# Performance work log

Hardware: AMD Instinct MI355X
Metric: run time of the kernel (lower is better)

Reference implementation:

```python
import math
import jax, jax.numpy as jnp
import numpy as np

# Frozen random shifts from the original module's __init__ (random.randint(-1,1))
SHIFT_C = 1   # p_2_0_1: roll along channel dim
SHIFT_H = 1   # p_4_1_0: roll along h
SHIFT_W = -1  # p_4_1_1: roll along w
K = 7         # horizontal window size (F.unfold kernel (1,7), padding (0,3))


def setup_inputs() -> dict:
    key = jax.random.key(0)
    k1, k2 = jax.random.split(key)
    n, c, h, w = 8, 256, 56, 56
    x = jax.random.normal(k1, (n, c, h, w), dtype=jnp.float32)
    # p_1_w ~ trunc_normal(std=0.1) around 1.0; approximate with 1 + 0.1*normal
    p1w = 1.0 + 0.1 * jax.random.normal(k2, (1, c, h, w), dtype=jnp.float32)
    return {"x": x, "p1w": p1w}


def _unfold_w7(t):
    # t: (n,c,h,w) -> (n,c,7,h,w): 7 horizontal taps, zero-padded (pad=3)
    w = t.shape[-1]
    tp = jnp.pad(t, ((0, 0), (0, 0), (0, 0), (3, 3)))
    return jnp.stack([tp[..., j:j + w] for j in range(K)], axis=2)


def reference(x, p1w):
    n, c, h, w = x.shape
    hw = h * w
    t1 = p1w * x                              # (n,c,h,w)
    t2 = jnp.roll(t1, SHIFT_C, axis=1)        # roll channels
    t3 = _unfold_w7(t2)                       # (n,c,7,h,w)
    t4 = jnp.roll(jnp.roll(t3, SHIFT_H, axis=3), SHIFT_W, axis=4)
    t5 = t1[:, :, None] - t3                  # (n,c,7,h,w)
    t6 = x[:, :, None] + t4                   # (n,c,7,h,w)
    x2 = x.reshape(n, c, hw)
    t5r = t5.reshape(n, c, K, hw)
    t6r = t6.reshape(n, c, K, hw)
    # scores: bmm(x (n,c,hw), t5^T (n,hw,c*7)) -> (n,c,c,7)
    t7 = jnp.einsum('nip,njkp->nijk', x2, t5r) / math.sqrt(hw)
    # aggregate: bmm(t7 (n,c,c*7), t6 (n,c*7,hw)) -> (n,c,hw)
    t8 = jnp.einsum('nijk,njkp->nip', t7, t6r) / math.sqrt(c * K)
    return t8.reshape(n, c, h, w)
```

## Files before the change

kernel.cpp:

```cpp
#include <hip/hip_runtime.h>

typedef unsigned short u16;
typedef __bf16 bf16x8 __attribute__((ext_vector_type(8)));
typedef float f32x4 __attribute__((ext_vector_type(4)));

#define HH  56
#define WW  56
#define HW  3136
#define CC  256
#define NB  8
#define CKP 2048
#define KS1 4
#define KS2 2

__device__ __forceinline__ u16 f2bf(float f) {
  unsigned int u = __float_as_uint(f);
  u += 0x7fffu + ((u >> 16) & 1u);
  return (u16)(u >> 16);
}
__device__ __forceinline__ float bf2f(u16 v) {
  return __uint_as_float((unsigned)v << 16);
}

__device__ __forceinline__ void lds_load16(const void* g, void* l) {
  __builtin_amdgcn_global_load_lds(
      (const __attribute__((address_space(1))) void*)g,
      (__attribute__((address_space(3))) void*)l, 16, 0, 0);
}

__global__ void pass1(const float* __restrict__ x, const float* __restrict__ p1w,
                      u16* __restrict__ t1b, u16* __restrict__ xb) {
  int i = blockIdx.x * 256 + threadIdx.x;
  int cw = i % (CC * HW / 4);
  float4 xv = ((const float4*)x)[i];
  float4 wv = ((const float4*)p1w)[cw];
  uint2 xo = make_uint2((unsigned)f2bf(xv.x) | ((unsigned)f2bf(xv.y) << 16),
                        (unsigned)f2bf(xv.z) | ((unsigned)f2bf(xv.w) << 16));
  ((uint2*)xb)[i] = xo;
  uint2 to = make_uint2((unsigned)f2bf(xv.x * wv.x) | ((unsigned)f2bf(xv.y * wv.y) << 16),
                        (unsigned)f2bf(xv.z * wv.z) | ((unsigned)f2bf(xv.w * wv.w) << 16));
  ((uint2*)t1b)[i] = to;
}

__global__ __launch_bounds__(256)
void gemm1f(const u16* __restrict__ A, const u16* __restrict__ t1b,
            float* __restrict__ Cp) {
  __shared__ u16 As[128 * 64];
  __shared__ u16 Bs[128 * 64];

  const int z = blockIdx.z, nb = z / KS1, ks = z % KS1;
  const int it0 = 49 * ks / KS1, it1 = 49 * (ks + 1) / KS1;
  const u16* Ab  = A   + (long)nb * CC * HW;
  const u16* t1n = t1b + (long)nb * CC * HW;
  const int m0 = blockIdx.x * 128, n0 = blockIdx.y * 128;
  const int jb = blockIdx.y * 16;
  const int t = threadIdx.x;
  const int lane = t & 63, wave = t >> 6;
  const int wm = wave & 1, wn = wave >> 1;
  const int lm = lane & 15, quad = lane >> 4;

  const int jl = (t >> 3) & 15, pc = t & 7, hf = t >> 7;
  const int j  = jb + jl;
  const int jm = (j + CC - 1) & (CC - 1);
  const u16* arow = t1n + (long)j  * HW;
  const u16* wrow = t1n + (long)jm * HW;

  f32x4 acc[4][4];
#pragma unroll
  for (int a = 0; a < 4; ++a)
#pragma unroll
    for (int b = 0; b < 4; ++b) acc[a][b] = (f32x4)0.0f;

  int rowc[4], colc[4];
#pragma unroll
  for (int ci = 0; ci < 4; ++ci) {
    int c = t + ci * 256;
    rowc[ci] = c >> 3;
    colc[ci] = ((c & 7) ^ (rowc[ci] & 7)) * 8;
  }

  for (int it = it0; it < it1; ++it) {
    const int k0 = it * 64;
#pragma unroll
    for (int ci = 0; ci < 4; ++ci)
      lds_load16(Ab + (long)(m0 + rowc[ci]) * HW + k0 + colc[ci],
                 &As[(t + ci * 256) * 8]);

    {
      const int p8 = k0 + pc * 8;
      u16 Ar[8], Wd[24];
      *(uint4*)Ar = *(const uint4*)&arow[p8];
#pragma unroll
      for (int L = 0; L < 3; ++L) {
        int ad = p8 - 8 + L * 8;
        ad = ad < 0 ? 0 : (ad > HW - 8 ? HW - 8 : ad);
        *(uint4*)&Wd[L * 8] = *(const uint4*)&wrow[ad];
      }
      int w0t = p8 % 56;
      float Af[8];
#pragma unroll
      for (int e = 0; e < 8; ++e) Af[e] = bf2f(Ar[e]);
      if (hf == 0) {
#pragma unroll
        for (int k = 0; k < 4; ++k) {
          u16 v[8];
#pragma unroll
          for (int e = 0; e < 8; ++e) {
            int w = w0t + e; if (w >= 56) w -= 56;
            float tap = ((unsigned)(w + k - 3) < 56u) ? bf2f(Wd[e + k + 5]) : 0.f;
            v[e] = f2bf(Af[e] - tap);
          }
          *(uint4*)&Bs[(jl * 8 + k) * 64 + (pc ^ k) * 8] = make_uint4(
              v[0] | ((unsigned)v[1] << 16), v[2] | ((unsigned)v[3] << 16),
              v[4] | ((unsigned)v[5] << 16), v[6] | ((unsigned)v[7] << 16));
        }
      } else {
#pragma unroll
        for (int k = 4; k < 7; ++k) {
          u16 v[8];
#pragma unroll
          for (int e = 0; e < 8; ++e) {
            int w = w0t + e; if (w >= 56) w -= 56;
            float tap = ((unsigned)(w + k - 3) < 56u) ? bf2f(Wd[e + k + 5]) : 0.f;
            v[e] = f2bf(Af[e] - tap);
          }
          *(uint4*)&Bs[(jl * 8 + k) * 64 + (pc ^ k) * 8] = make_uint4(
              v[0] | ((unsigned)v[1] << 16), v[2] | ((unsigned)v[3] << 16),
              v[4] | ((unsigned)v[5] << 16), v[6] | ((unsigned)v[7] << 16));
        }
        *(uint4*)&Bs[(jl * 8 + 7) * 64 + (pc ^ 7) * 8] = make_uint4(0, 0, 0, 0);
      }
    }
    __syncthreads();
#pragma unroll
    for (int kk = 0; kk < 2; ++kk) {
      const int phys = ((kk * 4 + quad) ^ (lm & 7)) * 8;
      bf16x8 af[4], bv[4];
#pragma unroll
      for (int mi = 0; mi < 4; ++mi)
        af[mi] = *(const bf16x8*)&As[(wm * 64 + mi * 16 + lm) * 64 + phys];
#pragma unroll
      for (int ni = 0; ni < 4; ++ni)
        bv[ni] = *(const bf16x8*)&Bs[(wn * 64 + ni * 16 + lm) * 64 + phys];
#pragma unroll
      for (int mi = 0; mi < 4; ++mi)
#pragma unroll
        for (int ni = 0; ni < 4; ++ni)
          acc[mi][ni] = __builtin_amdgcn_mfma_f32_16x16x32_bf16(
              af[mi], bv[ni], acc[mi][ni], 0, 0, 0);
    }
    __syncthreads();
  }

  float* Cb = Cp + ((long)ks * NB + nb) * (long)CC * CKP;
#pragma unroll
  for (int mi = 0; mi < 4; ++mi)
#pragma unroll
    for (int ni = 0; ni < 4; ++ni) {
      int rb = m0 + wm * 64 + mi * 16 + quad * 4;
      int cg = n0 + wn * 64 + ni * 16 + lm;
#pragma unroll
      for (int r = 0; r < 4; ++r)
        Cb[(long)(rb + r) * CKP + cg] = acc[mi][ni][r];
    }
}

__global__ void reduce1(const float* __restrict__ p1, u16* __restrict__ t7) {
  const int i = blockIdx.x * 256 + threadIdx.x;
  const long S = (long)NB * CC * CKP / 4;
  float4 a = ((const float4*)p1)[i];
  float4 b = ((const float4*)p1)[i + S];
  float4 c = ((const float4*)p1)[i + 2 * S];
  float4 d = ((const float4*)p1)[i + 3 * S];
  const float s = 1.0f / 56.0f;
  float e0 = (a.x + b.x + c.x + d.x) * s;
  float e1 = (a.y + b.y + c.y + d.y) * s;
  float e2 = (a.z + b.z + c.z + d.z) * s;
  float e3 = (a.w + b.w + c.w + d.w) * s;
  u16 w3 = (i & 1) ? (u16)0 : f2bf(e3);
  ushort4 o = make_ushort4(f2bf(e0), f2bf(e1), f2bf(e2), w3);
  ((ushort4*)t7)[i] = o;
}

__global__ __launch_bounds__(256)
void gemm2f(const u16* __restrict__ A, const u16* __restrict__ xb,
            const u16* __restrict__ t1b, float* __restrict__ Cp) {
  __shared__ u16 As[128 * 64];
  __shared__ u16 Bs[64 * 64];

  const int z = blockIdx.z, nb = z / KS2, ks = z % KS2;
  const int it0 = 16 * ks, it1 = 16 * (ks + 1);
  const u16* Ab  = A   + (long)nb * CC * CKP;
  const u16* xbn = xb  + (long)nb * CC * HW;
  const u16* t1n = t1b + (long)nb * CC * HW;
  const int m0 = blockIdx.x * 128, n0 = blockIdx.y * 64;
  const int t = threadIdx.x;
  const int lane = t & 63, wave = t >> 6;
  const int wm = wave & 1, wn = wave >> 1;
  const int lm = lane & 15, quad = lane >> 4;

  const int pr = t & 63, jg = t >> 6;
  const int p  = n0 + pr;
  const int h  = p / WW, w = p - h * WW;
  const int h2 = (h + HH - 1) % HH;
  const int w2 = (w + 1) % WW;
  const int swz = pr & 7;

  f32x4 acc[4][2];
#pragma unroll
  for (int a = 0; a < 4; ++a)
#pragma unroll
    for (int b = 0; b < 2; ++b) acc[a][b] = (f32x4)0.0f;

  int rowc[4], colc[4];
#pragma unroll
  for (int ci = 0; ci < 4; ++ci) {
    int c = t + ci * 256;
    rowc[ci] = c >> 3;
    colc[ci] = ((c & 7) ^ (rowc[ci] & 7)) * 8;
  }

  for (int it = it0; it < it1; ++it) {
    const int k0 = it * 64;
#pragma unroll
    for (int ci = 0; ci < 4; ++ci)
      lds_load16(Ab + (long)(m0 + rowc[ci]) * CKP + k0 + colc[ci],
                 &As[(t + ci * 256) * 8]);

#pragma unroll
    for (int jj = 0; jj < 2; ++jj) {
      const int jch = it * 8 + jg * 2 + jj;
      const int jmm = (jch + CC - 1) & (CC - 1);
      const float xv = bf2f(xbn[(long)jch * HW + p]);
      const u16* trow = t1n + (long)jmm * HW + h2 * WW;
      u16 v[8];
#pragma unroll
      for (int k = 0; k < 7; ++k) {
        int ww = w2 + k - 3;
        int wc = ww < 0 ? 0 : (ww > 55 ? 55 : ww);
        float tv = bf2f(trow[wc]);
        float tap = ((unsigned)ww < 56u) ? tv : 0.f;
        v[k] = f2bf(xv + tap);
      }
      v[7] = 0;
      *(uint4*)&Bs[pr * 64 + (((jg * 2 + jj) ^ swz) * 8)] = make_uint4(
          v[0] | ((unsigned)v[1] << 16), v[2] | ((unsigned)v[3] << 16),
          v[4] | ((unsigned)v[5] << 16), v[6] | ((unsigned)v[7] << 16));
    }
    __syncthreads();
#pragma unroll
    for (int kk = 0; kk < 2; ++kk) {
      const int phys = ((kk * 4 + quad) ^ (lm & 7)) * 8;
      bf16x8 af[4], bv[2];
#pragma unroll
      for (int mi = 0; mi < 4; ++mi)
        af[mi] = *(const bf16x8*)&As[(wm * 64 + mi * 16 + lm) * 64 + phys];
#pragma unroll
      for (int ni = 0; ni < 2; ++ni)
        bv[ni] = *(const bf16x8*)&Bs[(wn * 32 + ni * 16 + lm) * 64 + phys];
#pragma unroll
      for (int mi = 0; mi < 4; ++mi)
#pragma unroll
        for (int ni = 0; ni < 2; ++ni)
          acc[mi][ni] = __builtin_amdgcn_mfma_f32_16x16x32_bf16(
              af[mi], bv[ni], acc[mi][ni], 0, 0, 0);
    }
    __syncthreads();
  }

  float* Cb = Cp + ((long)ks * NB + nb) * (long)CC * HW;
#pragma unroll
  for (int mi = 0; mi < 4; ++mi)
#pragma unroll
    for (int ni = 0; ni < 2; ++ni) {
      int rb = m0 + wm * 64 + mi * 16 + quad * 4;
      int cg = n0 + wn * 32 + ni * 16 + lm;
#pragma unroll
      for (int r = 0; r < 4; ++r)
        Cb[(long)(rb + r) * HW + cg] = acc[mi][ni][r];
    }
}

__global__ void reduce2(const float* __restrict__ p2, float* __restrict__ out) {
  const int i = blockIdx.x * 256 + threadIdx.x;
  const long S = (long)NB * CC * HW / 4;
  float4 a = ((const float4*)p2)[i];
  float4 b = ((const float4*)p2)[i + S];
  const float s = 0.023622783f;
  float4 o;
  o.x = (a.x + b.x) * s; o.y = (a.y + b.y) * s;
  o.z = (a.z + b.z) * s; o.w = (a.w + b.w) * s;
  ((float4*)out)[i] = o;
}

extern "C" void kernel_launch(void* const* d_in, const int* in_sizes, int n_in,
                              void* d_out, int out_size, void* d_ws, size_t ws_size,
                              hipStream_t stream) {
  const float* x   = (const float*)d_in[0];
  const float* p1w = (const float*)d_in[1];

  char* ws = (char*)d_ws;
  size_t o = 0;
  u16* xb  = (u16*)(ws + o); o += (size_t)NB * CC * HW * 2;
  u16* t1b = (u16*)(ws + o); o += (size_t)NB * CC * HW * 2;
  u16* t7  = (u16*)(ws + o); o += (size_t)NB * CC * CKP * 2;
  float* p1 = (float*)(ws + o); o += (size_t)KS1 * NB * CC * CKP * 4;
  float* p2 = p1;

  pass1<<<NB * CC * HW / 4 / 256, 256, 0, stream>>>(x, p1w, t1b, xb);
  gemm1f<<<dim3(2, 16, NB * KS1), 256, 0, stream>>>(xb, t1b, p1);
  reduce1<<<NB * CC * CKP / 4 / 256, 256, 0, stream>>>(p1, t7);
  gemm2f<<<dim3(2, 49, NB * KS2), 256, 0, stream>>>(t7, xb, t1b, p2);
  reduce2<<<NB * CC * HW / 4 / 256, 256, 0, stream>>>(p2, (float*)d_out);
}
```

Measured before the change: 216.0 us.

## Double-buffer generated B tiles and read A fragments directly from global

Both GEMM kernels now keep the on-the-fly generated B operand in a double-buffered LDS tile. The next tile is generated after the current MFMA step, so only one barrier per iteration is needed and generation can overlap the matrix math. The A operand is no longer staged through LDS with global_load_lds; each wave loads its bf16x8 fragments straight from global memory. This frees LDS and removes the staging traffic, but risks uncoalesced, repeated global reads of A across the waves that share rows, relying on L1/L2 caches.

```diff
diff --git a/kernel.cpp b/kernel.cpp
--- a/kernel.cpp
+++ b/kernel.cpp
@@ -20,12 +20,6 @@
 }
 __device__ __forceinline__ float bf2f(u16 v) {
   return __uint_as_float((unsigned)v << 16);
-}
-
-__device__ __forceinline__ void lds_load16(const void* g, void* l) {
-  __builtin_amdgcn_global_load_lds(
-      (const __attribute__((address_space(1))) void*)g,
-      (__attribute__((address_space(3))) void*)l, 16, 0, 0);
 }
 
 __global__ void pass1(const float* __restrict__ x, const float* __restrict__ p1w,
@@ -45,8 +39,7 @@
 __global__ __launch_bounds__(256)
 void gemm1f(const u16* __restrict__ A, const u16* __restrict__ t1b,
             float* __restrict__ Cp) {
-  __shared__ u16 As[128 * 64];
-  __shared__ u16 Bs[128 * 64];
+  __shared__ u16 Bs[2 * 128 * 64];
 
   const int z = blockIdx.z, nb = z / KS1, ks = z % KS1;
   const int it0 = 49 * ks / KS1, it1 = 49 * (ks + 1) / KS1;
@@ -71,77 +64,71 @@
 #pragma unroll
     for (int b = 0; b < 4; ++b) acc[a][b] = (f32x4)0.0f;
 
-  int rowc[4], colc[4];
-#pragma unroll
-  for (int ci = 0; ci < 4; ++ci) {
-    int c = t + ci * 256;
-    rowc[ci] = c >> 3;
-    colc[ci] = ((c & 7) ^ (rowc[ci] & 7)) * 8;
-  }
+  auto genB = [&](int it, int buf) {
+    const int k0 = it * 64;
+    const int p8 = k0 + pc * 8;
+    u16* Bp = &Bs[buf * 8192];
+    u16 Ar[8], Wd[24];
+    *(uint4*)Ar = *(const uint4*)&arow[p8];
+#pragma unroll
+    for (int L = 0; L < 3; ++L) {
+      int ad = p8 - 8 + L * 8;
+      ad = ad < 0 ? 0 : (ad > HW - 8 ? HW - 8 : ad);
+      *(uint4*)&Wd[L * 8] = *(const uint4*)&wrow[ad];
+    }
+    int w0t = p8 % 56;
+    float Af[8];
+#pragma unroll
+    for (int e = 0; e < 8; ++e) Af[e] = bf2f(Ar[e]);
+    if (hf == 0) {
+#pragma unroll
+      for (int k = 0; k < 4; ++k) {
+        u16 v[8];
+#pragma unroll
+        for (int e = 0; e < 8; ++e) {
+          int w = w0t + e; if (w >= 56) w -= 56;
+          float tap = ((unsigned)(w + k - 3) < 56u) ? bf2f(Wd[e + k + 5]) : 0.f;
+          v[e] = f2bf(Af[e] - tap);
+        }
+        *(uint4*)&Bp[(jl * 8 + k) * 64 + (pc ^ k) * 8] = make_uint4(
+            v[0] | ((unsigned)v[1] << 16), v[2] | ((unsigned)v[3] << 16),
+            v[4] | ((unsigned)v[5] << 16), v[6] | ((unsigned)v[7] << 16));
+      }
+    } else {
+#pragma unroll
+      for (int k = 4; k < 7; ++k) {
+        u16 v[8];
+#pragma unroll
+        for (int e = 0; e < 8; ++e) {
+          int w = w0t + e; if (w >= 56) w -= 56;
+          float tap = ((unsigned)(w + k - 3) < 56u) ? bf2f(Wd[e + k + 5]) : 0.f;
+          v[e] = f2bf(Af[e] - tap);
+        }
+        *(uint4*)&Bp[(jl * 8 + k) * 64 + (pc ^ k) * 8] = make_uint4(
+            v[0] | ((unsigned)v[1] << 16), v[2] | ((unsigned)v[3] << 16),
+            v[4] | ((unsigned)v[5] << 16), v[6] | ((unsigned)v[7] << 16));
+      }
+      *(uint4*)&Bp[(jl * 8 + 7) * 64 + (pc ^ 7) * 8] = make_uint4(0, 0, 0, 0);
+    }
+  };
+
+  genB(it0, 0);
+  __syncthreads();
 
   for (int it = it0; it < it1; ++it) {
     const int k0 = it * 64;
-#pragma unroll
-    for (int ci = 0; ci < 4; ++ci)
-      lds_load16(Ab + (long)(m0 + rowc[ci]) * HW + k0 + colc[ci],
-                 &As[(t + ci * 256) * 8]);
-
-    {
-      const int p8 = k0 + pc * 8;
-      u16 Ar[8], Wd[24];
-      *(uint4*)Ar = *(const uint4*)&arow[p8];
-#pragma unroll
-      for (int L = 0; L < 3; ++L) {
-        int ad = p8 - 8 + L * 8;
-        ad = ad < 0 ? 0 : (ad > HW - 8 ? HW - 8 : ad);
-        *(uint4*)&Wd[L * 8] = *(const uint4*)&wrow[ad];
-      }
-      int w0t = p8 % 56;
-      float Af[8];
-#pragma unroll
-      for (int e = 0; e < 8; ++e) Af[e] = bf2f(Ar[e]);
-      if (hf == 0) {
-#pragma unroll
-        for (int k = 0; k < 4; ++k) {
-          u16 v[8];
-#pragma unroll
-          for (int e = 0; e < 8; ++e) {
-            int w = w0t + e; if (w >= 56) w -= 56;
-            float tap = ((unsigned)(w + k - 3) < 56u) ? bf2f(Wd[e + k + 5]) : 0.f;
-            v[e] = f2bf(Af[e] - tap);
-          }
-          *(uint4*)&Bs[(jl * 8 + k) * 64 + (pc ^ k) * 8] = make_uint4(
-              v[0] | ((unsigned)v[1] << 16), v[2] | ((unsigned)v[3] << 16),
-              v[4] | ((unsigned)v[5] << 16), v[6] | ((unsigned)v[7] << 16));
-        }
-      } else {
-#pragma unroll
-        for (int k = 4; k < 7; ++k) {
-          u16 v[8];
-#pragma unroll
-          for (int e = 0; e < 8; ++e) {
-            int w = w0t + e; if (w >= 56) w -= 56;
-            float tap = ((unsigned)(w + k - 3) < 56u) ? bf2f(Wd[e + k + 5]) : 0.f;
-            v[e] = f2bf(Af[e] - tap);
-          }
-          *(uint4*)&Bs[(jl * 8 + k) * 64 + (pc ^ k) * 8] = make_uint4(
-              v[0] | ((unsigned)v[1] << 16), v[2] | ((unsigned)v[3] << 16),
-              v[4] | ((unsigned)v[5] << 16), v[6] | ((unsigned)v[7] << 16));
-        }
-        *(uint4*)&Bs[(jl * 8 + 7) * 64 + (pc ^ 7) * 8] = make_uint4(0, 0, 0, 0);
-      }
-    }
-    __syncthreads();
+    const int cb = (it - it0) & 1;
 #pragma unroll
     for (int kk = 0; kk < 2; ++kk) {
       const int phys = ((kk * 4 + quad) ^ (lm & 7)) * 8;
       bf16x8 af[4], bv[4];
 #pragma unroll
       for (int mi = 0; mi < 4; ++mi)
-        af[mi] = *(const bf16x8*)&As[(wm * 64 + mi * 16 + lm) * 64 + phys];
+        af[mi] = *(const bf16x8*)&Ab[(long)(m0 + wm * 64 + mi * 16 + lm) * HW
+                                     + k0 + (kk * 4 + quad) * 8];
 #pragma unroll
       for (int ni = 0; ni < 4; ++ni)
-        bv[ni] = *(const bf16x8*)&Bs[(wn * 64 + ni * 16 + lm) * 64 + phys];
+        bv[ni] = *(const bf16x8*)&Bs[cb * 8192 + (wn * 64 + ni * 16 + lm) * 64 + phys];
 #pragma unroll
       for (int mi = 0; mi < 4; ++mi)
 #pragma unroll
@@ -149,6 +136,8 @@
           acc[mi][ni] = __builtin_amdgcn_mfma_f32_16x16x32_bf16(
               af[mi], bv[ni], acc[mi][ni], 0, 0, 0);
     }
+    int itn = it + 1 < it1 ? it + 1 : it;
+    genB(itn, cb ^ 1);
     __syncthreads();
   }
 
@@ -185,8 +174,7 @@
 __global__ __launch_bounds__(256)
 void gemm2f(const u16* __restrict__ A, const u16* __restrict__ xb,
             const u16* __restrict__ t1b, float* __restrict__ Cp) {
-  __shared__ u16 As[128 * 64];
-  __shared__ u16 Bs[64 * 64];
+  __shared__ u16 Bs[2 * 64 * 64];
 
   const int z = blockIdx.z, nb = z / KS2, ks = z % KS2;
   const int it0 = 16 * ks, it1 = 16 * (ks + 1);
@@ -212,21 +200,8 @@
 #pragma unroll
     for (int b = 0; b < 2; ++b) acc[a][b] = (f32x4)0.0f;
 
-  int rowc[4], colc[4];
-#pragma unroll
-  for (int ci = 0; ci < 4; ++ci) {
-    int c = t + ci * 256;
-    rowc[ci] = c >> 3;
-    colc[ci] = ((c & 7) ^ (rowc[ci] & 7)) * 8;
-  }
-
-  for (int it = it0; it < it1; ++it) {
-    const int k0 = it * 64;
-#pragma unroll
-    for (int ci = 0; ci < 4; ++ci)
-      lds_load16(Ab + (long)(m0 + rowc[ci]) * CKP + k0 + colc[ci],
-                 &As[(t + ci * 256) * 8]);
-
+  auto genB = [&](int it, int buf) {
+    u16* Bp = &Bs[buf * 4096];
 #pragma unroll
     for (int jj = 0; jj < 2; ++jj) {
       const int jch = it * 8 + jg * 2 + jj;
@@ -243,21 +218,29 @@
         v[k] = f2bf(xv + tap);
       }
       v[7] = 0;
-      *(uint4*)&Bs[pr * 64 + (((jg * 2 + jj) ^ swz) * 8)] = make_uint4(
+      *(uint4*)&Bp[pr * 64 + (((jg * 2 + jj) ^ swz) * 8)] = make_uint4(
           v[0] | ((unsigned)v[1] << 16), v[2] | ((unsigned)v[3] << 16),
           v[4] | ((unsigned)v[5] << 16), v[6] | ((unsigned)v[7] << 16));
     }
-    __syncthreads();
+  };
+
+  genB(it0, 0);
+  __syncthreads();
+
+  for (int it = it0; it < it1; ++it) {
+    const int k0 = it * 64;
+    const int cb = (it - it0) & 1;
 #pragma unroll
     for (int kk = 0; kk < 2; ++kk) {
       const int phys = ((kk * 4 + quad) ^ (lm & 7)) * 8;
       bf16x8 af[4], bv[2];
 #pragma unroll
       for (int mi = 0; mi < 4; ++mi)
-        af[mi] = *(const bf16x8*)&As[(wm * 64 + mi * 16 + lm) * 64 + phys];
+        af[mi] = *(const bf16x8*)&Ab[(long)(m0 + wm * 64 + mi * 16 + lm) * CKP
+                                     + k0 + (kk * 4 + quad) * 8];
 #pragma unroll
       for (int ni = 0; ni < 2; ++ni)
-        bv[ni] = *(const bf16x8*)&Bs[(wn * 32 + ni * 16 + lm) * 64 + phys];
+        bv[ni] = *(const bf16x8*)&Bs[cb * 4096 + (wn * 32 + ni * 16 + lm) * 64 + phys];
 #pragma unroll
       for (int mi = 0; mi < 4; ++mi)
 #pragma unroll
@@ -265,6 +248,8 @@
           acc[mi][ni] = __builtin_amdgcn_mfma_f32_16x16x32_bf16(
               af[mi], bv[ni], acc[mi][ni], 0, 0, 0);
     }
+    int itn = it + 1 < it1 ? it + 1 : it;
+    genB(itn, cb ^ 1);
     __syncthreads();
   }
 
```

Measured after the change: 327.8 us. 1.52x slower.
